# Kernel optimization log

Measured on AMD Instinct MI355X. Metric: run time of the kernel, lower is better.

The kernel has to match this reference:

```python
import jax, jax.numpy as jnp
import numpy as np

B, C, H, W = 4, 64, 256, 256
ALPHA_LOW = 0.8   # approx phase blend
ALPHA_HIGH = 0.4  # detail mag/phase blend
PI = float(np.pi)


def setup_inputs() -> dict:
    key = jax.random.key(0)
    names = ["content_approx", "content_h", "content_v", "content_d",
             "style_approx", "style_h", "style_v", "style_d"]
    keys = jax.random.split(key, len(names))
    return {n: jax.random.normal(k, (B, C, H, W), dtype=jnp.float32)
            for n, k in zip(names, keys)}


def _phase(x):
    # torch.angle(x.to(complex64)) for real x: pi where x<0, else 0
    return jnp.where(x < 0, jnp.asarray(PI, x.dtype), jnp.asarray(0.0, x.dtype))


def _hist_match(src, tgt):
    # Per-(batch,channel) histogram matching. src/tgt: [B,C,H,W].
    # Equal lengths => np.interp over matched linspaces is identity, so
    # mapped = sort(tgt) scattered by argsort(src), i.e. gather by rank of src.
    shp = src.shape
    s = src.reshape(-1, shp[-2] * shp[-1])   # [B*C, H*W]
    t = tgt.reshape(-1, shp[-2] * shp[-1])
    order = jnp.argsort(s, axis=-1)
    rank = jnp.argsort(order, axis=-1)       # inverse permutation (rank of each elem)
    t_sorted = jnp.sort(t, axis=-1)
    return jnp.take_along_axis(t_sorted, rank, axis=-1).reshape(shp)


def _process_detail(c, s, alpha):
    blended_mag = alpha * jnp.abs(c) + (1.0 - alpha) * jnp.abs(s)
    blended_phase = alpha * _phase(c) + (1.0 - alpha) * _phase(s)
    return blended_mag * jnp.cos(blended_phase)  # polar(mag, phase).real


def reference(content_approx, content_h, content_v, content_d,
              style_approx, style_h, style_v, style_d):
    # Approx band: histogram-matched magnitude (detached in original) + blended phase
    matched_mag = jax.lax.stop_gradient(
        _hist_match(jnp.abs(content_approx), jnp.abs(style_approx)))
    blended_phase = ALPHA_LOW * _phase(content_approx) + (1.0 - ALPHA_LOW) * _phase(style_approx)
    stylized_approx = matched_mag * jnp.cos(blended_phase)
    stylized_h = _process_detail(content_h, style_h, ALPHA_HIGH)
    stylized_v = _process_detail(content_v, style_v, ALPHA_HIGH)
    stylized_d = _process_detail(content_d, style_d, ALPHA_HIGH)
    return (stylized_approx, stylized_h, stylized_v, stylized_d)
```

## Files before the change

kernel.cpp:

```cpp
#include <hip/hip_runtime.h>
#include <cstdint>

namespace {

constexpr int ROWS = 256;
constexpr int ROW_N = 65536;
constexpr int ST = 1024;
constexpr int CHUNK = 4096;
constexpr int NCHUNK = ROW_N / CHUNK;
constexpr int SUBS = 64;
constexpr int EPT = 4;
constexpr size_t NTOT = (size_t)ROWS * ROW_N;

constexpr float COS_02PI = 0.80901699437494745f;
constexpr float COS_04PI = 0.30901699437494745f;

struct SortSmem {
    __align__(16) uint16_t whist[SUBS * 256];
    __align__(16) uint32_t stage[CHUNK];
    __align__(16) uint8_t  dstg[CHUNK];
    __align__(16) uint32_t hist[256];
    uint32_t sbase[2][256];
    uint32_t adj[2][256];
    uint32_t wavesum[4];
};

__device__ __forceinline__ uint32_t fkey(float x) {
    return __float_as_uint(fabsf(x));
}

__device__ void prepass_hist(SortSmem& sm, const float* __restrict__ rawA)
{
    const int tid = threadIdx.x;
    const float4* r4 = (const float4*)rawA;
#pragma unroll 4
    for (int i = 0; i < ROW_N / 4 / ST; ++i) {
        float4 f = r4[i * ST + tid];
        atomicAdd(&sm.hist[(fkey(f.x) >> 10) & 255u], 1u);
        atomicAdd(&sm.hist[(fkey(f.y) >> 10) & 255u], 1u);
        atomicAdd(&sm.hist[(fkey(f.z) >> 10) & 255u], 1u);
        atomicAdd(&sm.hist[(fkey(f.w) >> 10) & 255u], 1u);
    }
    __syncthreads();
}

template <bool IS_SRC, int P>
__device__ void run_pass(SortSmem& sm, const float* __restrict__ rawA,
                         const float* __restrict__ rawS,
                         const uint32_t* __restrict__ inBuf,
                         uint32_t* __restrict__ outBuf)
{
    constexpr int DBITS = (P == 0) ? 8 : 7;
    constexpr int ND = 1 << DBITS;
    constexpr int DSH = (P == 0) ? 10 : (P == 1 ? 18 : 25);
    constexpr bool P0SRC = IS_SRC && (P == 0);

    const int tid = threadIdx.x;
    const int lane = tid & 63;
    const int wave = tid >> 6;
    const uint64_t lane_lt = (1ull << lane) - 1ull;

    {
        uint32_t h = 0u, incl = 0u;
        if (tid < ND) {
            h = sm.hist[tid];
            sm.hist[tid] = 0u;
            incl = h;
#pragma unroll
            for (int dd = 1; dd < 64; dd <<= 1) {
                uint32_t t = __shfl_up(incl, dd, 64);
                if (lane >= dd) incl += t;
            }
            if (lane == 63) sm.wavesum[tid >> 6] = incl;
        }
        __syncthreads();
        if (tid < ND) {
            uint32_t woff = 0u;
#pragma unroll
            for (int j = 0; j < ND / 64; ++j)
                if (j < (tid >> 6)) woff += sm.wavesum[j];
            sm.sbase[0][tid] = woff + incl - h;
        }
        __syncthreads();
    }

    auto loadE = [&](int c, int k) -> uint2 {
        const int pos = c * CHUNK + (k << 10) + (wave << 6) + lane;
        if constexpr (P == 0) {
            float av = rawA[pos];
            uint32_t kk = fkey(av);
            if constexpr (IS_SRC) {
                float sv = rawS[pos];
                uint32_t o = ((kk >> 18) << 18) | (uint32_t)pos;
                if (av < 0.f) o |= 1u << 16;
                if (sv < 0.f) o |= 1u << 17;
                return make_uint2(o, (kk >> 10) & 255u);
            } else {
                return make_uint2(kk, (kk >> 10) & 255u);
            }
        } else {
            uint32_t v = inBuf[pos];
            return make_uint2(v, (v >> DSH) & (ND - 1));
        }
    };

    uint2 e[EPT];
#pragma unroll
    for (int k = 0; k < EPT; ++k) e[k] = loadE(0, k);

    for (int c = 0; c < NCHUNK; ++c) {
        const int par = c & 1;

        {
            uint4 z = make_uint4(0u, 0u, 0u, 0u);
#pragma unroll
            for (int k = 0; k < EPT; ++k) {
                uint4* rp = (uint4*)&sm.whist[(k * 16 + wave) * ND];
                if (lane < ND / 8) rp[lane] = z;
            }
        }

        uint32_t rw[EPT];
#pragma unroll
        for (int k = 0; k < EPT; ++k) {
            const uint32_t d = e[k].y;
            uint64_t m = ~0ull;
#pragma unroll
            for (int b = 0; b < DBITS; ++b) {
                uint64_t bal = __ballot((d >> b) & 1u);
                m &= ((d >> b) & 1u) ? bal : ~bal;
            }
            rw[k] = (uint32_t)__popcll(m & lane_lt);
            if (rw[k] == 0u)
                sm.whist[(k * 16 + wave) * ND + d] = (uint16_t)__popcll(m);
        }

        if constexpr (P == 0) {
#pragma unroll
            for (int k = 0; k < EPT; ++k)
                atomicAdd(&sm.hist[(e[k].x >> 18) & 127u], 1u);
        } else if constexpr (P == 1) {
#pragma unroll
            for (int k = 0; k < EPT; ++k) {
                const uint32_t nd = (e[k].x >> 25) & 127u;
                uint64_t m = ~0ull;
#pragma unroll
                for (int b = 0; b < 7; ++b) {
                    uint64_t bal = __ballot((nd >> b) & 1u);
                    m &= ((nd >> b) & 1u) ? bal : ~bal;
                }
                if ((m & lane_lt) == 0ull)
                    atomicAdd(&sm.hist[nd], (uint32_t)__popcll(m));
            }
        }
        __syncthreads();

        uint32_t tot = 0u, incl = 0u;
        if (tid < ND) {
#pragma unroll
            for (int s = 0; s < SUBS; ++s) tot += sm.whist[s * ND + tid];
            incl = tot;
#pragma unroll
            for (int dd = 1; dd < 64; dd <<= 1) {
                uint32_t t = __shfl_up(incl, dd, 64);
                if (lane >= dd) incl += t;
            }
            if (lane == 63) sm.wavesum[tid >> 6] = incl;
        }
        __syncthreads();

        if (tid < ND) {
            uint32_t woff = 0u;
#pragma unroll
            for (int j = 0; j < ND / 64; ++j)
                if (j < (tid >> 6)) woff += sm.wavesum[j];
            const uint32_t ls = woff + incl - tot;
            uint32_t run = ls;
#pragma unroll
            for (int s = 0; s < SUBS; ++s) {
                uint32_t t = sm.whist[s * ND + tid];
                sm.whist[s * ND + tid] = (uint16_t)run;
                run += t;
            }
            const uint32_t sb = sm.sbase[par][tid];
            sm.adj[par][tid] = sb - ls;
            sm.sbase[par ^ 1][tid] = sb + (run - ls);
        }
        __syncthreads();

#pragma unroll
        for (int k = 0; k < EPT; ++k) {
            const uint32_t s = (uint32_t)sm.whist[(k * 16 + wave) * ND + e[k].y]
                               + rw[k];
            sm.stage[s] = e[k].x;
            if constexpr (P0SRC) sm.dstg[s] = (uint8_t)e[k].y;
        }
        uint2 n[EPT];
#pragma unroll
        for (int k = 0; k < EPT; ++k) n[k] = make_uint2(0u, 0u);
        if (c + 1 < NCHUNK) {
#pragma unroll
            for (int k = 0; k < EPT; ++k) n[k] = loadE(c + 1, k);
        }
        __syncthreads();

#pragma unroll
        for (int h = 0; h < EPT; ++h) {
            const int slot = tid + (h << 10);
            const uint32_t u = sm.stage[slot];
            uint32_t d;
            if constexpr (P0SRC) d = sm.dstg[slot];
            else                 d = (u >> DSH) & (ND - 1);
            const uint32_t go = sm.adj[par][d] + (uint32_t)slot;
            uint32_t ov = u;
            if constexpr (IS_SRC && P == 2) ov = u & 0x3FFFFu;
            outBuf[go] = ov;
        }
#pragma unroll
        for (int k = 0; k < EPT; ++k) e[k] = n[k];
    }
    __syncthreads();
}

__device__ __forceinline__ float detail_one(float c, float s) {
    const float f = (c < 0.f) ? ((s < 0.f) ? -1.f : COS_04PI)
                              : ((s < 0.f) ? -COS_04PI : 1.f);
    return (0.4f * fabsf(c) + 0.6f * fabsf(s)) * f;
}

}

__global__ __launch_bounds__(ST, 8)
void sort_kernel(const float* __restrict__ ca, const float* __restrict__ sa,
                 uint32_t* srcA, uint32_t* srcB,
                 uint32_t* tgtA, uint32_t* tgtB, uint32_t* tgtF)
{
    __shared__ SortSmem sm;
    const int row = blockIdx.x >> 1;
    if (threadIdx.x < 256) sm.hist[threadIdx.x] = 0u;
    __syncthreads();

    if ((blockIdx.x & 1) == 0) {
        const float* cRow = ca + (size_t)row * ROW_N;
        const float* sRow = sa + (size_t)row * ROW_N;
        uint32_t* A = srcA + (size_t)row * ROW_N;
        uint32_t* B = srcB + (size_t)row * ROW_N;
        prepass_hist(sm, cRow);
        run_pass<true, 0>(sm, cRow, sRow, nullptr, A);
        run_pass<true, 1>(sm, nullptr, nullptr, A, B);
        run_pass<true, 2>(sm, nullptr, nullptr, B, A);
    } else {
        const float* sRow = sa + (size_t)row * ROW_N;
        uint32_t* A = tgtA + (size_t)row * ROW_N;
        uint32_t* B = tgtB + (size_t)row * ROW_N;
        uint32_t* F = tgtF + (size_t)row * ROW_N;
        prepass_hist(sm, sRow);
        run_pass<false, 0>(sm, sRow, nullptr, nullptr, A);
        run_pass<false, 1>(sm, nullptr, nullptr, A, B);
        run_pass<false, 2>(sm, nullptr, nullptr, B, F);
    }
}

__global__ __launch_bounds__(256)
void approx_finalize(const uint32_t* __restrict__ srcF,
                     const uint32_t* __restrict__ tgtF,
                     float* __restrict__ out0)
{
    const size_t kk = (size_t)blockIdx.x * blockDim.x + threadIdx.x;
    const uint32_t v = srcF[kk];
    const size_t j = ((kk >> 16) << 16) | (v & 0xFFFFu);
    const float t = __uint_as_float(tgtF[kk]);
    const uint32_t cneg = (v >> 16) & 1u;
    const uint32_t sneg = (v >> 17) & 1u;
    const float f = cneg ? (sneg ? -1.f : -COS_02PI)
                         : (sneg ? COS_02PI : 1.f);
    out0[j] = t * f;
}

__global__ __launch_bounds__(256)
void details_kernel(const float4* __restrict__ ch, const float4* __restrict__ sh,
                    const float4* __restrict__ cv, const float4* __restrict__ sv,
                    const float4* __restrict__ cd, const float4* __restrict__ sd,
                    float4* __restrict__ oh, float4* __restrict__ ov,
                    float4* __restrict__ od)
{
    const size_t i = (size_t)blockIdx.x * blockDim.x + threadIdx.x;
    float4 a, b, r;
    a = ch[i]; b = sh[i];
    r.x = detail_one(a.x, b.x); r.y = detail_one(a.y, b.y);
    r.z = detail_one(a.z, b.z); r.w = detail_one(a.w, b.w);
    oh[i] = r;
    a = cv[i]; b = sv[i];
    r.x = detail_one(a.x, b.x); r.y = detail_one(a.y, b.y);
    r.z = detail_one(a.z, b.z); r.w = detail_one(a.w, b.w);
    ov[i] = r;
    a = cd[i]; b = sd[i];
    r.x = detail_one(a.x, b.x); r.y = detail_one(a.y, b.y);
    r.z = detail_one(a.z, b.z); r.w = detail_one(a.w, b.w);
    od[i] = r;
}

extern "C" void kernel_launch(void* const* d_in, const int* in_sizes, int n_in,
                              void* d_out, int out_size, void* d_ws, size_t ws_size,
                              hipStream_t stream)
{
    (void)in_sizes; (void)n_in; (void)out_size; (void)ws_size;
    const float* ca = (const float*)d_in[0];
    const float* ch = (const float*)d_in[1];
    const float* cv = (const float*)d_in[2];
    const float* cd = (const float*)d_in[3];
    const float* sa = (const float*)d_in[4];
    const float* sh = (const float*)d_in[5];
    const float* sv = (const float*)d_in[6];
    const float* sd = (const float*)d_in[7];

    float* out = (float*)d_out;
    float* out_a = out;
    float* out_h = out + NTOT;
    float* out_v = out + 2 * NTOT;
    float* out_d = out + 3 * NTOT;

    uint32_t* srcA = (uint32_t*)d_ws;
    uint32_t* srcB = (uint32_t*)((char*)d_ws + NTOT * 4);
    uint32_t* tgtA = (uint32_t*)out_d;
    uint32_t* tgtB = (uint32_t*)out_h;
    uint32_t* tgtF = (uint32_t*)out_v;

    sort_kernel<<<2 * ROWS, ST, 0, stream>>>(ca, sa, srcA, srcB, tgtA, tgtB, tgtF);

    approx_finalize<<<(int)(NTOT / 256), 256, 0, stream>>>(
        (const uint32_t*)srcA, (const uint32_t*)tgtF, out_a);

    details_kernel<<<(int)(NTOT / 4 / 256), 256, 0, stream>>>(
        (const float4*)ch, (const float4*)sh,
        (const float4*)cv, (const float4*)sv,
        (const float4*)cd, (const float4*)sd,
        (float4*)out_h, (float4*)out_v, (float4*)out_d);
}
```

Measured before the change: 626.8 us.

## Parallelize radix-sort digit scan across subgroups and fuse epilogue kernels

The per-digit scan over 64 sub-histograms, previously done serially by one thread per digit, is split into four groups of 16. The groups are reduced in parallel, prefix-combined, then rescanned in parallel, at the cost of extra barriers and shared memory. The approx finalize and details kernels are merged into one persistent-style kernel with 2048 blocks that loop over rows and float4 chunks, which removes a launch and changes the access order of the scatter. The target's final sorted buffer moves from the out_v output into workspace so the fused kernel does not read memory it overwrites. This needs a larger workspace.

```diff
diff --git a/kernel.cpp b/kernel.cpp
--- a/kernel.cpp
+++ b/kernel.cpp
@@ -12,6 +12,8 @@
 constexpr int EPT = 4;
 constexpr size_t NTOT = (size_t)ROWS * ROW_N;
 
+constexpr int EB = 2048;
+
 constexpr float COS_02PI = 0.80901699437494745f;
 constexpr float COS_04PI = 0.30901699437494745f;
 
@@ -20,6 +22,8 @@
     __align__(16) uint32_t stage[CHUNK];
     __align__(16) uint8_t  dstg[CHUNK];
     __align__(16) uint32_t hist[256];
+    __align__(16) uint32_t gpart[4 * 256];
+    __align__(16) uint32_t gbase[4 * 256];
     uint32_t sbase[2][256];
     uint32_t adj[2][256];
     uint32_t wavesum[4];
@@ -155,10 +159,20 @@
         }
         __syncthreads();
 
+        if (tid < ND * 4) {
+            const int d = tid & (ND - 1), g = tid >> DBITS;
+            uint32_t gs = 0u;
+#pragma unroll
+            for (int s = 0; s < 16; ++s)
+                gs += sm.whist[((g << 4) + s) * ND + d];
+            sm.gpart[(g << DBITS) + d] = gs;
+        }
+        __syncthreads();
+
         uint32_t tot = 0u, incl = 0u;
         if (tid < ND) {
-#pragma unroll
-            for (int s = 0; s < SUBS; ++s) tot += sm.whist[s * ND + tid];
+            tot = sm.gpart[tid] + sm.gpart[ND + tid]
+                + sm.gpart[2 * ND + tid] + sm.gpart[3 * ND + tid];
             incl = tot;
 #pragma unroll
             for (int dd = 1; dd < 64; dd <<= 1) {
@@ -175,16 +189,27 @@
             for (int j = 0; j < ND / 64; ++j)
                 if (j < (tid >> 6)) woff += sm.wavesum[j];
             const uint32_t ls = woff + incl - tot;
-            uint32_t run = ls;
-#pragma unroll
-            for (int s = 0; s < SUBS; ++s) {
-                uint32_t t = sm.whist[s * ND + tid];
-                sm.whist[s * ND + tid] = (uint16_t)run;
-                run += t;
-            }
+            uint32_t r0 = ls;
+            sm.gbase[tid] = r0;            r0 += sm.gpart[tid];
+            sm.gbase[ND + tid] = r0;       r0 += sm.gpart[ND + tid];
+            sm.gbase[2 * ND + tid] = r0;   r0 += sm.gpart[2 * ND + tid];
+            sm.gbase[3 * ND + tid] = r0;
             const uint32_t sb = sm.sbase[par][tid];
             sm.adj[par][tid] = sb - ls;
-            sm.sbase[par ^ 1][tid] = sb + (run - ls);
+            sm.sbase[par ^ 1][tid] = sb + tot;
+        }
+        __syncthreads();
+
+        if (tid < ND * 4) {
+            const int d = tid & (ND - 1), g = tid >> DBITS;
+            uint32_t run = sm.gbase[(g << DBITS) + d];
+#pragma unroll
+            for (int s = 0; s < 16; ++s) {
+                const int wi = ((g << 4) + s) * ND + d;
+                uint32_t t2 = sm.whist[wi];
+                sm.whist[wi] = (uint16_t)run;
+                run += t2;
+            }
         }
         __syncthreads();
 
@@ -262,42 +287,48 @@
 }
 
 __global__ __launch_bounds__(256)
-void approx_finalize(const uint32_t* __restrict__ srcF,
+void epilogue_kernel(const uint32_t* __restrict__ srcF,
                      const uint32_t* __restrict__ tgtF,
-                     float* __restrict__ out0)
-{
-    const size_t kk = (size_t)blockIdx.x * blockDim.x + threadIdx.x;
-    const uint32_t v = srcF[kk];
-    const size_t j = ((kk >> 16) << 16) | (v & 0xFFFFu);
-    const float t = __uint_as_float(tgtF[kk]);
-    const uint32_t cneg = (v >> 16) & 1u;
-    const uint32_t sneg = (v >> 17) & 1u;
-    const float f = cneg ? (sneg ? -1.f : -COS_02PI)
-                         : (sneg ? COS_02PI : 1.f);
-    out0[j] = t * f;
-}
-
-__global__ __launch_bounds__(256)
-void details_kernel(const float4* __restrict__ ch, const float4* __restrict__ sh,
-                    const float4* __restrict__ cv, const float4* __restrict__ sv,
-                    const float4* __restrict__ cd, const float4* __restrict__ sd,
-                    float4* __restrict__ oh, float4* __restrict__ ov,
-                    float4* __restrict__ od)
-{
-    const size_t i = (size_t)blockIdx.x * blockDim.x + threadIdx.x;
-    float4 a, b, r;
-    a = ch[i]; b = sh[i];
-    r.x = detail_one(a.x, b.x); r.y = detail_one(a.y, b.y);
-    r.z = detail_one(a.z, b.z); r.w = detail_one(a.w, b.w);
-    oh[i] = r;
-    a = cv[i]; b = sv[i];
-    r.x = detail_one(a.x, b.x); r.y = detail_one(a.y, b.y);
-    r.z = detail_one(a.z, b.z); r.w = detail_one(a.w, b.w);
-    ov[i] = r;
-    a = cd[i]; b = sd[i];
-    r.x = detail_one(a.x, b.x); r.y = detail_one(a.y, b.y);
-    r.z = detail_one(a.z, b.z); r.w = detail_one(a.w, b.w);
-    od[i] = r;
+                     const float4* __restrict__ ch, const float4* __restrict__ sh,
+                     const float4* __restrict__ cv, const float4* __restrict__ sv,
+                     const float4* __restrict__ cd, const float4* __restrict__ sd,
+                     float* __restrict__ out0,
+                     float4* __restrict__ oh, float4* __restrict__ ov,
+                     float4* __restrict__ od)
+{
+    const int b = blockIdx.x, t = threadIdx.x;
+    const int x = b & 7, j = b >> 3;
+
+    for (int i = 0; i < 32; ++i) {
+        const int row = x + (i << 3);
+        const size_t kk = ((size_t)row << 16) + (size_t)((j << 8) + t);
+        const uint32_t v = srcF[kk];
+        const float tv = __uint_as_float(tgtF[kk]);
+        const uint32_t cneg = (v >> 16) & 1u;
+        const uint32_t sneg = (v >> 17) & 1u;
+        const float f = cneg ? (sneg ? -1.f : -COS_02PI)
+                             : (sneg ? COS_02PI : 1.f);
+        out0[((size_t)row << 16) | (v & 0xFFFFu)] = tv * f;
+    }
+
+    const size_t base = (size_t)(b << 8) + t;
+#pragma unroll
+    for (int it = 0; it < 8; ++it) {
+        const size_t i4 = (size_t)it * (EB * 256) + base;
+        float4 a, bb, r;
+        a = ch[i4]; bb = sh[i4];
+        r.x = detail_one(a.x, bb.x); r.y = detail_one(a.y, bb.y);
+        r.z = detail_one(a.z, bb.z); r.w = detail_one(a.w, bb.w);
+        oh[i4] = r;
+        a = cv[i4]; bb = sv[i4];
+        r.x = detail_one(a.x, bb.x); r.y = detail_one(a.y, bb.y);
+        r.z = detail_one(a.z, bb.z); r.w = detail_one(a.w, bb.w);
+        ov[i4] = r;
+        a = cd[i4]; bb = sd[i4];
+        r.x = detail_one(a.x, bb.x); r.y = detail_one(a.y, bb.y);
+        r.z = detail_one(a.z, bb.z); r.w = detail_one(a.w, bb.w);
+        od[i4] = r;
+    }
 }
 
 extern "C" void kernel_launch(void* const* d_in, const int* in_sizes, int n_in,
@@ -322,18 +353,16 @@
 
     uint32_t* srcA = (uint32_t*)d_ws;
     uint32_t* srcB = (uint32_t*)((char*)d_ws + NTOT * 4);
+    uint32_t* tgtF = (uint32_t*)((char*)d_ws + NTOT * 8);
     uint32_t* tgtA = (uint32_t*)out_d;
     uint32_t* tgtB = (uint32_t*)out_h;
-    uint32_t* tgtF = (uint32_t*)out_v;
 
     sort_kernel<<<2 * ROWS, ST, 0, stream>>>(ca, sa, srcA, srcB, tgtA, tgtB, tgtF);
 
-    approx_finalize<<<(int)(NTOT / 256), 256, 0, stream>>>(
-        (const uint32_t*)srcA, (const uint32_t*)tgtF, out_a);
-
-    details_kernel<<<(int)(NTOT / 4 / 256), 256, 0, stream>>>(
+    epilogue_kernel<<<EB, 256, 0, stream>>>(
+        (const uint32_t*)srcA, (const uint32_t*)tgtF,
         (const float4*)ch, (const float4*)sh,
         (const float4*)cv, (const float4*)sv,
         (const float4*)cd, (const float4*)sd,
-        (float4*)out_h, (float4*)out_v, (float4*)out_d);
-}
+        out_a, (float4*)out_h, (float4*)out_v, (float4*)out_d);
+}
```

New measurement: 698.1 us. 11.4% more time.

## Use LDS atomic ranking in radix sort with smaller chunks, move tgtF to workspace

Applied to the files above, without the earlier changes.

Per-wave digit ranking now uses LDS atomicAdd on 32-bit per-wave histograms instead of ballot-based match masks, with chunk size, subhistogram count and elements per thread halved to fit the wider histograms. The final target buffer moves from an output slot to workspace, and the details kernel uses ext_vector_type float4. Atomics remove the per-bit ballot loop but add LDS atomic contention. Atomic return order is nondeterministic within a wave, so the sort may lose stability.

```diff
diff --git a/kernel.cpp b/kernel.cpp
--- a/kernel.cpp
+++ b/kernel.cpp
@@ -6,17 +6,19 @@
 constexpr int ROWS = 256;
 constexpr int ROW_N = 65536;
 constexpr int ST = 1024;
-constexpr int CHUNK = 4096;
+constexpr int CHUNK = 2048;
 constexpr int NCHUNK = ROW_N / CHUNK;
-constexpr int SUBS = 64;
-constexpr int EPT = 4;
+constexpr int SUBS = 32;
+constexpr int EPT = 2;
 constexpr size_t NTOT = (size_t)ROWS * ROW_N;
 
 constexpr float COS_02PI = 0.80901699437494745f;
 constexpr float COS_04PI = 0.30901699437494745f;
 
+typedef float f4v __attribute__((ext_vector_type(4)));
+
 struct SortSmem {
-    __align__(16) uint16_t whist[SUBS * 256];
+    __align__(16) uint32_t whist[SUBS * 256];
     __align__(16) uint32_t stage[CHUNK];
     __align__(16) uint8_t  dstg[CHUNK];
     __align__(16) uint32_t hist[256];
@@ -116,24 +118,14 @@
 #pragma unroll
             for (int k = 0; k < EPT; ++k) {
                 uint4* rp = (uint4*)&sm.whist[(k * 16 + wave) * ND];
-                if (lane < ND / 8) rp[lane] = z;
-            }
-        }
-
-        uint32_t rw[EPT];
-#pragma unroll
-        for (int k = 0; k < EPT; ++k) {
-            const uint32_t d = e[k].y;
-            uint64_t m = ~0ull;
-#pragma unroll
-            for (int b = 0; b < DBITS; ++b) {
-                uint64_t bal = __ballot((d >> b) & 1u);
-                m &= ((d >> b) & 1u) ? bal : ~bal;
-            }
-            rw[k] = (uint32_t)__popcll(m & lane_lt);
-            if (rw[k] == 0u)
-                sm.whist[(k * 16 + wave) * ND + d] = (uint16_t)__popcll(m);
-        }
+                if (lane < ND / 4) rp[lane] = z;
+            }
+        }
+
+        uint32_t rk[EPT];
+#pragma unroll
+        for (int k = 0; k < EPT; ++k)
+            rk[k] = atomicAdd(&sm.whist[(k * 16 + wave) * ND + e[k].y], 1u);
 
         if constexpr (P == 0) {
 #pragma unroll
@@ -179,19 +171,18 @@
 #pragma unroll
             for (int s = 0; s < SUBS; ++s) {
                 uint32_t t = sm.whist[s * ND + tid];
-                sm.whist[s * ND + tid] = (uint16_t)run;
+                sm.whist[s * ND + tid] = run;
                 run += t;
             }
             const uint32_t sb = sm.sbase[par][tid];
             sm.adj[par][tid] = sb - ls;
-            sm.sbase[par ^ 1][tid] = sb + (run - ls);
+            sm.sbase[par ^ 1][tid] = sb + tot;
         }
         __syncthreads();
 
 #pragma unroll
         for (int k = 0; k < EPT; ++k) {
-            const uint32_t s = (uint32_t)sm.whist[(k * 16 + wave) * ND + e[k].y]
-                               + rw[k];
+            const uint32_t s = sm.whist[(k * 16 + wave) * ND + e[k].y] + rk[k];
             sm.stage[s] = e[k].x;
             if constexpr (P0SRC) sm.dstg[s] = (uint8_t)e[k].y;
         }
@@ -278,14 +269,14 @@
 }
 
 __global__ __launch_bounds__(256)
-void details_kernel(const float4* __restrict__ ch, const float4* __restrict__ sh,
-                    const float4* __restrict__ cv, const float4* __restrict__ sv,
-                    const float4* __restrict__ cd, const float4* __restrict__ sd,
-                    float4* __restrict__ oh, float4* __restrict__ ov,
-                    float4* __restrict__ od)
+void details_kernel(const f4v* __restrict__ ch, const f4v* __restrict__ sh,
+                    const f4v* __restrict__ cv, const f4v* __restrict__ sv,
+                    const f4v* __restrict__ cd, const f4v* __restrict__ sd,
+                    f4v* __restrict__ oh, f4v* __restrict__ ov,
+                    f4v* __restrict__ od)
 {
     const size_t i = (size_t)blockIdx.x * blockDim.x + threadIdx.x;
-    float4 a, b, r;
+    f4v a, b, r;
     a = ch[i]; b = sh[i];
     r.x = detail_one(a.x, b.x); r.y = detail_one(a.y, b.y);
     r.z = detail_one(a.z, b.z); r.w = detail_one(a.w, b.w);
@@ -322,18 +313,17 @@
 
     uint32_t* srcA = (uint32_t*)d_ws;
     uint32_t* srcB = (uint32_t*)((char*)d_ws + NTOT * 4);
+    uint32_t* tgtF = (uint32_t*)((char*)d_ws + NTOT * 8);
     uint32_t* tgtA = (uint32_t*)out_d;
     uint32_t* tgtB = (uint32_t*)out_h;
-    uint32_t* tgtF = (uint32_t*)out_v;
 
     sort_kernel<<<2 * ROWS, ST, 0, stream>>>(ca, sa, srcA, srcB, tgtA, tgtB, tgtF);
 
-    approx_finalize<<<(int)(NTOT / 256), 256, 0, stream>>>(
-        (const uint32_t*)srcA, (const uint32_t*)tgtF, out_a);
+    approx_finalize<<<(int)(NTOT / 256), 256, 0, stream>>>(srcA, tgtF, out_a);
 
     details_kernel<<<(int)(NTOT / 4 / 256), 256, 0, stream>>>(
-        (const float4*)ch, (const float4*)sh,
-        (const float4*)cv, (const float4*)sv,
-        (const float4*)cd, (const float4*)sd,
-        (float4*)out_h, (float4*)out_v, (float4*)out_d);
-}
+        (const f4v*)ch, (const f4v*)sh,
+        (const f4v*)cv, (const f4v*)sv,
+        (const f4v*)cd, (const f4v*)sd,
+        (f4v*)out_h, (f4v*)out_v, (f4v*)out_d);
+}
```

Measured after the change: 634.1 us. No clear change (+1.2%).
